# Performance work log

Measured on AMD Instinct MI355X. Metric: run time of the kernel, lower is better.

Reference implementation:

```python
import jax, jax.numpy as jnp
import numpy as np

B, F, H, W, C = 1, 16, 32, 32, 128


def setup_inputs() -> dict:
    key = jax.random.key(0)
    ks = jax.random.split(key, 6)
    w = lambda k: jax.random.normal(k, (C, C), jnp.float32) * 0.02
    return {
        "x": jax.random.normal(ks[0], (B, F, H, W, C), jnp.float32),
        "gamma": jnp.ones((C,), jnp.float32),
        "wq": w(ks[1]), "bq": jnp.zeros((C,), jnp.float32),
        "wk": w(ks[2]), "bk": jnp.zeros((C,), jnp.float32),
        "wv": w(ks[3]), "bv": jnp.zeros((C,), jnp.float32),
        "wo": w(ks[4]), "bo": jnp.zeros((C,), jnp.float32),
    }


def reference(x, gamma, wq, bq, wk, bk, wv, bv, wo, bo):
    b, f, h, w_, c = x.shape
    s, n_hw = f * h * w_, h * w_
    identity = x

    # RMSNorm variant: L2-normalize over channels, rescale by sqrt(C) * gamma
    xn = x / (jnp.linalg.norm(x, axis=-1, keepdims=True) + 1e-8)
    xn = xn * (c ** 0.5) * gamma

    # 1x1x1 convs == pointwise linear projections; flatten to tokens [b, s, c]
    xn = xn.reshape(b, s, c)
    q = xn @ wq + bq
    k = xn @ wk + bk
    v = xn @ wv + bv

    # frame-causal block mask: query at frame i attends to all keys in frames <= i
    frame = jnp.arange(s) // n_hw                      # [s]
    allowed = frame[:, None] >= frame[None, :]          # [s, s] bool

    scale = 1.0 / jnp.sqrt(c)
    scores = jnp.einsum('bqc,bkc->bqk', q, k) * scale   # [b, s, s]
    scores = jnp.where(allowed, scores, -jnp.inf)
    attn = jax.nn.softmax(scores, axis=-1)
    out = jnp.einsum('bqk,bkc->bqc', attn, v)           # [b, s, c]

    out = out @ wo + bo
    return out.reshape(b, f, h, w_, c) + identity
```

## Files before the change

### kernel.cpp

```cpp
#include <hip/hip_runtime.h>
#include <hip/hip_bf16.h>

typedef __bf16 bf16x8 __attribute__((ext_vector_type(8)));
typedef float f32x4 __attribute__((ext_vector_type(4)));
typedef float f32x16 __attribute__((ext_vector_type(16)));
typedef unsigned short u16;
typedef unsigned int u32;
typedef u16 ushort8 __attribute__((ext_vector_type(8)));
typedef u32 u32x4 __attribute__((ext_vector_type(4)));

#define S_TOK 16384
#define C_DIM 128
#define L2E 1.4426950408889634f
#define QK_SCALE 0.08838834764831845f
#define SQRTC 11.313708498984761f

#define NBLK 512
#define TPB 34

#define WT_OFF   0u
#define BIAS_OFF 131072u
#define XN_OFF   147456u
#define O_OFF    XN_OFF
#define Q_OFF    (XN_OFF + 4194304u)
#define K_OFF    (Q_OFF + 4194304u)
#define VF_OFF   (K_OFF + 4194304u)
#define PART_OFF (VF_OFF + 4194304u)
#define ML_OFF   (PART_OFF + 20971520u)

#define ZERO16 ((f32x16){0.f,0.f,0.f,0.f,0.f,0.f,0.f,0.f,0.f,0.f,0.f,0.f,0.f,0.f,0.f,0.f})

__device__ __forceinline__ int in_is_bf16(const void* gamma) {
  return ((const u16*)gamma)[0] == 0x3F80;
}
__device__ __forceinline__ float ldf(const void* p, int i, int bf) {
  if (bf) { u32 b = ((const u16*)p)[i]; return __uint_as_float(b << 16); }
  return ((const float*)p)[i];
}
__device__ __forceinline__ float b2f(u16 b) { return __uint_as_float((u32)b << 16); }
__device__ __forceinline__ u16 f2b(float f) {
  return __builtin_bit_cast(u16, (__bf16)f);
}
__device__ __forceinline__ float fexp2(float x) {
  float y; asm("v_exp_f32 %0, %1" : "=v"(y) : "v"(x)); return y;
}
__device__ __forceinline__ void gld16(const void* g, void* l) {
  __builtin_amdgcn_global_load_lds((const __attribute__((address_space(1))) u32*)g,
                                   (__attribute__((address_space(3))) u32*)l, 16, 0, 0);
}
__device__ __forceinline__ int qb_of(int t) {
  int F = 0;
  while (64 * (F + 1) * (F + 2) <= t) F++;
  int span = 16 * (F + 1);
  return 8 * F + (t - 64 * F * (F + 1)) / span;
}
__device__ __forceinline__ int start_of(int qq) {
  int Fq = qq >> 3, iq = qq & 7;
  return 16 * (Fq + 1) * (4 * Fq + iq);
}

__global__ void __launch_bounds__(256) prep_norm_kernel(const void* x, const void* gamma,
    const void* wq, const void* bq, const void* wk, const void* bk,
    const void* wv, const void* bv, const void* wo, const void* bo, char* ws) {
  int bf = in_is_bf16(gamma);
  if (blockIdx.x >= 2048) {
    int bb = blockIdx.x - 2048;
    if (bb < 256) {
      int gid = bb * 256 + threadIdx.x;
      int m = gid >> 14; int rem = gid & 16383;
      int k = rem >> 7; int n = rem & 127;
      const void* W = (m == 0) ? wq : (m == 1) ? wk : (m == 2) ? wv : wo;
      float v = ldf(W, rem, bf);
      if (m == 0) v *= QK_SCALE;
      *(u16*)(ws + WT_OFF + (u32)m * 32768u + (u32)n * 256u + (((u32)k * 2u) ^ (u32)((n & 7) << 4))) = f2b(v);
    } else {
      int idx = (bb - 256) * 256 + threadIdx.x;
      if (idx < 512) {
        int m = idx >> 7; int c = idx & 127;
        const void* B = (m == 0) ? bq : (m == 1) ? bk : (m == 2) ? bv : bo;
        float v = ldf(B, c, bf);
        if (m == 0) v *= QK_SCALE;
        ((float*)(ws + BIAS_OFF))[idx] = v;
      }
    }
    return;
  }
  int t = blockIdx.x * 256 + threadIdx.x;
  int tok = t >> 5; int sub = t & 31;
  int base = tok * 128 + sub * 4;
  float f[4];
  if (bf) {
    ushort4 v = ((const ushort4*)x)[base >> 2];
    f[0] = __uint_as_float((u32)v.x << 16); f[1] = __uint_as_float((u32)v.y << 16);
    f[2] = __uint_as_float((u32)v.z << 16); f[3] = __uint_as_float((u32)v.w << 16);
  } else {
    float4 v = ((const float4*)x)[base >> 2];
    f[0] = v.x; f[1] = v.y; f[2] = v.z; f[3] = v.w;
  }
  float ss = f[0]*f[0] + f[1]*f[1] + f[2]*f[2] + f[3]*f[3];
  #pragma unroll
  for (int m = 1; m < 32; m <<= 1) ss += __shfl_xor(ss, m);
  float fac = SQRTC / (sqrtf(ss) + 1e-8f);
  u16 o[4];
  #pragma unroll
  for (int j = 0; j < 4; j++) { float g = ldf(gamma, sub * 4 + j, bf); o[j] = f2b(f[j] * fac * g); }
  *(ushort4*)(ws + XN_OFF + (u32)tok * 256u + (((u32)sub * 8u) ^ (u32)((tok & 7) << 4))) =
      make_ushort4(o[0], o[1], o[2], o[3]);
}

__global__ void __launch_bounds__(256) qkv_kernel(char* ws) {
  __shared__ char lds[65536];
  int tid = threadIdx.x; int wid = tid >> 6; int lane = tid & 63;
  int blk = blockIdx.x & 127;
  int m = blockIdx.x >> 7;
  #pragma unroll
  for (int i = 0; i < 8; i++) {
    u32 seg = (u32)(i * 4 + wid) * 1024u;
    gld16(ws + XN_OFF + (u32)blk * 32768u + seg + (u32)lane * 16u, lds + seg);
    gld16(ws + WT_OFF + (u32)m * 32768u + seg + (u32)lane * 16u, lds + 32768 + seg);
  }
  __syncthreads();
  const float* bias = (const float*)(ws + BIAS_OFF);
  int rb = wid * 32;
  f32x4 acc[2][8];
  #pragma unroll
  for (int a = 0; a < 2; a++)
    #pragma unroll
    for (int b = 0; b < 8; b++) acc[a][b] = (f32x4){0.f, 0.f, 0.f, 0.f};
  #pragma unroll
  for (int kt = 0; kt < 4; kt++) {
    bf16x8 afr[2];
    #pragma unroll
    for (int mt = 0; mt < 2; mt++) {
      int row = rb + mt * 16 + (lane & 15);
      afr[mt] = *(const bf16x8*)(lds + row * 256 + ((kt * 64 + ((lane >> 4) * 16)) ^ ((row & 7) << 4)));
    }
    #pragma unroll
    for (int nt = 0; nt < 8; nt++) {
      int nr = nt * 16 + (lane & 15);
      bf16x8 bfr = *(const bf16x8*)(lds + 32768 + nr * 256 + ((kt * 64 + ((lane >> 4) * 16)) ^ ((nr & 7) << 4)));
      #pragma unroll
      for (int mt = 0; mt < 2; mt++)
        acc[mt][nt] = __builtin_amdgcn_mfma_f32_16x16x32_bf16(afr[mt], bfr, acc[mt][nt], 0, 0, 0);
    }
  }
  #pragma unroll
  for (int mt = 0; mt < 2; mt++)
    #pragma unroll
    for (int nt = 0; nt < 8; nt++) {
      int tok0 = blk * 128 + rb + mt * 16 + (lane >> 4) * 4;
      int c = (lane & 15) + nt * 16;
      float bv_ = bias[m * 128 + c];
      if (m == 0) {
        #pragma unroll
        for (int r = 0; r < 4; r++)
          *(u16*)(ws + Q_OFF + ((u32)(tok0 + r) * 128u + (u32)c) * 2u) = f2b(acc[mt][nt][r] + bv_);
      } else if (m == 1) {
        char* bp = ws + K_OFF + (u32)(tok0 >> 6) * 16384u
                 + (u32)((((tok0 >> 5) & 1) << 3) + (c >> 4)) * 1024u
                 + (u32)((tok0 & 31) + 32 * ((c >> 3) & 1)) * 16u + (u32)(c & 7) * 2u;
        #pragma unroll
        for (int r = 0; r < 4; r++)
          *(u16*)(bp + r * 16) = f2b(acc[mt][nt][r] + bv_);
      } else {
        u16 pk[4];
        #pragma unroll
        for (int r = 0; r < 4; r++) pk[r] = f2b(acc[mt][nt][r] + bv_);
        *(ushort4*)(ws + VF_OFF + (u32)(tok0 >> 6) * 16384u
                    + (u32)(((c >> 5) << 2) + ((tok0 >> 4) & 3)) * 1024u
                    + (u32)((c & 31) + 32 * ((tok0 >> 3) & 1)) * 16u + (u32)(tok0 & 7) * 2u)
            = make_ushort4(pk[0], pk[1], pk[2], pk[3]);
      }
    }
}

__global__ void __launch_bounds__(256, 2) attn_part_kernel(char* ws) {
  __shared__ char lds[65536];
  int tid = threadIdx.x; int wid = tid >> 6; int lane = tid & 63;
  int q = lane & 31; int hi = lane >> 5;
  int b = blockIdx.x;
  int slot = b;
  for (int qq = 1; qq < 128; qq++) {
    int Sx = start_of(qq);
    if (Sx < TPB * b && (Sx % TPB) != 0) slot++;
  }
  ushort8 ones_u;
  #pragma unroll
  for (int e = 0; e < 8; e++) ones_u[e] = 0x3F80;
  bf16x8 ones = __builtin_bit_cast(bf16x8, ones_u);

  auto stageK = [&](int t, int buf) {
    #pragma unroll
    for (int i = 0; i < 4; i++) {
      u32 off = (u32)(i * 4096) + (u32)tid * 16u;
      gld16(ws + K_OFF + (u32)t * 16384u + off, lds + buf * 16384 + off);
    }
  };
  auto stageV = [&](int t, int buf) {
    #pragma unroll
    for (int i = 0; i < 4; i++) {
      u32 off = (u32)(i * 4096) + (u32)tid * 16u;
      gld16(ws + VF_OFF + (u32)t * 16384u + off, lds + 32768 + buf * 16384 + off);
    }
  };

  int t0 = TPB * b, remaining = TPB;
  while (remaining > 0) {
    int F = 0;
    while (64 * (F + 1) * (F + 2) <= t0) F++;
    int fb = 64 * F * (F + 1); int span = 16 * (F + 1);
    int i = (t0 - fb) / span; int l = t0 - fb - i * span;
    int qb = 8 * F + i;
    int nt = min(remaining, span - l);

    bf16x8 aq[8];
    {
      const char* qp = ws + Q_OFF + (u32)(qb * 128 + wid * 32 + q) * 256u + (u32)(hi * 16);
      #pragma unroll
      for (int kt = 0; kt < 8; kt++) aq[kt] = *(const bf16x8*)(qp + kt * 32);
    }
    f32x16 acc0 = ZERO16, acc1 = ZERO16, acc2 = ZERO16, acc3 = ZERO16, accl = ZERO16;
    float m_run = -1e30f;
    float mL2 = m_run * L2E;

    __syncthreads();
    stageK(l, 0); stageV(l, 0);
    for (int it = 0; it < nt; it++) {
      int cur = it & 1;
      __syncthreads();
      if (it + 1 < nt) { stageK(l + it + 1, cur ^ 1); stageV(l + it + 1, cur ^ 1); }
      const char* kb_ = lds + cur * 16384;
      const char* vb_ = lds + 32768 + cur * 16384;
      f32x16 s0 = ZERO16, s1 = ZERO16;
      __builtin_amdgcn_s_setprio(1);
      #pragma unroll
      for (int kt = 0; kt < 8; kt++) {
        bf16x8 k0 = *(const bf16x8*)(kb_ + (0 * 8 + kt) * 1024 + (u32)lane * 16u);
        bf16x8 k1 = *(const bf16x8*)(kb_ + (1 * 8 + kt) * 1024 + (u32)lane * 16u);
        s0 = __builtin_amdgcn_mfma_f32_32x32x16_bf16(k0, aq[kt], s0, 0, 0, 0);
        s1 = __builtin_amdgcn_mfma_f32_32x32x16_bf16(k1, aq[kt], s1, 0, 0, 0);
      }
      __builtin_amdgcn_s_setprio(0);
      float tm = s0[0];
      #pragma unroll
      for (int r = 1; r < 16; r++) tm = fmaxf(tm, s0[r]);
      #pragma unroll
      for (int r = 0; r < 16; r++) tm = fmaxf(tm, s1[r]);
      tm = fmaxf(tm, __shfl_xor(tm, 32));
      if (__any(tm > m_run + 8.0f)) {
        float mnew = fmaxf(m_run, tm);
        float alpha = fexp2((m_run - mnew) * L2E);
        #pragma unroll
        for (int r = 0; r < 16; r++) {
          acc0[r] *= alpha; acc1[r] *= alpha; acc2[r] *= alpha; acc3[r] *= alpha; accl[r] *= alpha;
        }
        m_run = mnew; mL2 = m_run * L2E;
      }
      u32 W[16];
      #pragma unroll
      for (int t = 0; t < 8; t++) {
        float pa = fexp2(__builtin_fmaf(s0[2 * t], L2E, -mL2));
        float pb = fexp2(__builtin_fmaf(s0[2 * t + 1], L2E, -mL2));
        asm("v_cvt_pk_bf16_f32 %0, %1, %2" : "=v"(W[t]) : "v"(pa), "v"(pb));
      }
      #pragma unroll
      for (int t = 0; t < 8; t++) {
        float pa = fexp2(__builtin_fmaf(s1[2 * t], L2E, -mL2));
        float pb = fexp2(__builtin_fmaf(s1[2 * t + 1], L2E, -mL2));
        asm("v_cvt_pk_bf16_f32 %0, %1, %2" : "=v"(W[8 + t]) : "v"(pa), "v"(pb));
      }
      __builtin_amdgcn_s_setprio(1);
      #pragma unroll
      for (int kq = 0; kq < 4; kq++) {
        int base = (kq >> 1) * 8 + (kq & 1) * 4;
        u32 e0 = W[base + 0], e2 = W[base + 2];
        u32 e1 = W[base + 1], e3 = W[base + 3];
        asm("v_permlane32_swap_b32 %0, %1" : "+v"(e2), "+v"(e0));
        asm("v_permlane32_swap_b32 %0, %1" : "+v"(e3), "+v"(e1));
        u32x4 pw = (u32x4){e0, e1, e2, e3};
        bf16x8 pfr = __builtin_bit_cast(bf16x8, pw);
        accl = __builtin_amdgcn_mfma_f32_32x32x16_bf16(ones, pfr, accl, 0, 0, 0);
        bf16x8 v0 = *(const bf16x8*)(vb_ + (0 * 4 + kq) * 1024 + (u32)lane * 16u);
        bf16x8 v1 = *(const bf16x8*)(vb_ + (1 * 4 + kq) * 1024 + (u32)lane * 16u);
        bf16x8 v2 = *(const bf16x8*)(vb_ + (2 * 4 + kq) * 1024 + (u32)lane * 16u);
        bf16x8 v3 = *(const bf16x8*)(vb_ + (3 * 4 + kq) * 1024 + (u32)lane * 16u);
        acc0 = __builtin_amdgcn_mfma_f32_32x32x16_bf16(v0, pfr, acc0, 0, 0, 0);
        acc1 = __builtin_amdgcn_mfma_f32_32x32x16_bf16(v1, pfr, acc1, 0, 0, 0);
        acc2 = __builtin_amdgcn_mfma_f32_32x32x16_bf16(v2, pfr, acc2, 0, 0, 0);
        acc3 = __builtin_amdgcn_mfma_f32_32x32x16_bf16(v3, pfr, acc3, 0, 0, 0);
      }
      __builtin_amdgcn_s_setprio(0);
    }
    float l_run = accl[0];
    float rinv = 1.0f / l_run;
    int lrow = wid * 32 + q;
    char* pb2 = ws + PART_OFF + (u32)slot * 32768u + (u32)lrow * 256u;
    #pragma unroll
    for (int cb = 0; cb < 4; cb++) {
      const f32x16* A = (cb == 0) ? &acc0 : (cb == 1) ? &acc1 : (cb == 2) ? &acc2 : &acc3;
      #pragma unroll
      for (int t = 0; t < 8; t++) {
        float fa = (*A)[2 * t] * rinv, fb = (*A)[2 * t + 1] * rinv;
        u32 w;
        asm("v_cvt_pk_bf16_f32 %0, %1, %2" : "=v"(w) : "v"(fa), "v"(fb));
        int ch = cb * 32 + 8 * (t >> 1) + 2 * (t & 1) + 4 * hi;
        *(u32*)(pb2 + ch * 2) = w;
      }
    }
    if (hi == 0) ((float2*)(ws + ML_OFF))[slot * 128 + lrow] = make_float2(m_run, l_run);
    t0 += nt; remaining -= nt; slot++;
  }
}

__global__ void __launch_bounds__(256) combine_kernel(char* ws) {
  int qb = blockIdx.x >> 2;
  int seg = blockIdx.x & 3;
  int Sq = start_of(qb);
  int Eq = Sq + 16 * ((qb >> 3) + 1);
  int c_lo = Sq / TPB, c_hi = (Eq - 1) / TPB;
  int bse0 = c_lo;
  for (int qq = 1; qq < 128; qq++) {
    int Sx = start_of(qq);
    if (Sx < TPB * c_lo && (Sx % TPB) != 0) bse0++;
  }
  int tid = threadIdx.x;
  int row = seg * 32 + (tid >> 3);
  int oct = tid & 7;
  const float2* ml = (const float2*)(ws + ML_OFF);
  float M = -1e30f;
  {
    int bse = bse0;
    for (int c = c_lo; c <= c_hi; c++) {
      int qbf = qb_of(TPB * c);
      int qbl = qb_of(TPB * c + TPB - 1);
      int slot = bse + (qb - qbf);
      M = fmaxf(M, ml[slot * 128 + row].x);
      bse += qbl - qbf + 1;
    }
  }
  float a[16];
  #pragma unroll
  for (int k = 0; k < 16; k++) a[k] = 0.f;
  float D = 0.f;
  {
    int bse = bse0;
    for (int c = c_lo; c <= c_hi; c++) {
      int qbf = qb_of(TPB * c);
      int qbl = qb_of(TPB * c + TPB - 1);
      int slot = bse + (qb - qbf);
      bse += qbl - qbf + 1;
      float2 m_l = ml[slot * 128 + row];
      float w = exp2f((m_l.x - M) * L2E) * m_l.y;
      D += w;
      const u16* o = (const u16*)(ws + PART_OFF + (u32)slot * 32768u + (u32)row * 256u + (u32)oct * 32u);
      ushort8 v0 = *(const ushort8*)o;
      ushort8 v1 = *(const ushort8*)(o + 8);
      #pragma unroll
      for (int e = 0; e < 8; e++) { a[e] += w * b2f(v0[e]); a[8 + e] += w * b2f(v1[e]); }
    }
  }
  float Dinv = 1.0f / D;
  int grow = qb * 128 + row;
  ushort8 w0, w1;
  #pragma unroll
  for (int e = 0; e < 8; e++) { w0[e] = f2b(a[e] * Dinv); w1[e] = f2b(a[8 + e] * Dinv); }
  u32 rbase = (u32)grow * 256u;
  u32 swz = (u32)((row & 7) << 4);
  *(ushort8*)(ws + O_OFF + rbase + (((u32)oct * 32u) ^ swz)) = w0;
  *(ushort8*)(ws + O_OFF + rbase + (((u32)oct * 32u + 16u) ^ swz)) = w1;
}

__global__ void __launch_bounds__(256) out_kernel(const void* x, const void* gamma, char* ws, void* out) {
  __shared__ char lds[65536];
  int bf = in_is_bf16(gamma);
  int tid = threadIdx.x; int wid = tid >> 6; int lane = tid & 63;
  int blk = blockIdx.x;
  #pragma unroll
  for (int i = 0; i < 8; i++) {
    u32 seg = (u32)(i * 4 + wid) * 1024u;
    gld16(ws + O_OFF + (u32)blk * 32768u + seg + (u32)lane * 16u, lds + seg);
    gld16(ws + WT_OFF + 3u * 32768u + seg + (u32)lane * 16u, lds + 32768 + seg);
  }
  __syncthreads();
  f32x4 acc[2][8];
  #pragma unroll
  for (int a = 0; a < 2; a++)
    #pragma unroll
    for (int b = 0; b < 8; b++) acc[a][b] = (f32x4){0.f, 0.f, 0.f, 0.f};
  int rb = wid * 32;
  #pragma unroll
  for (int kt = 0; kt < 4; kt++) {
    bf16x8 afr[2];
    #pragma unroll
    for (int mt = 0; mt < 2; mt++) {
      int row = rb + mt * 16 + (lane & 15);
      afr[mt] = *(const bf16x8*)(lds + row * 256 + ((kt * 64 + ((lane >> 4) * 16)) ^ ((row & 7) << 4)));
    }
    #pragma unroll
    for (int nt = 0; nt < 8; nt++) {
      int nr = nt * 16 + (lane & 15);
      bf16x8 bfr = *(const bf16x8*)(lds + 32768 + nr * 256 + ((kt * 64 + ((lane >> 4) * 16)) ^ ((nr & 7) << 4)));
      #pragma unroll
      for (int mt = 0; mt < 2; mt++)
        acc[mt][nt] = __builtin_amdgcn_mfma_f32_16x16x32_bf16(afr[mt], bfr, acc[mt][nt], 0, 0, 0);
    }
  }
  const float* bias = (const float*)(ws + BIAS_OFF) + 3 * 128;
  #pragma unroll
  for (int mt = 0; mt < 2; mt++)
    #pragma unroll
    for (int nt = 0; nt < 8; nt++) {
      int c = (lane & 15) + nt * 16;
      float bv_ = bias[c];
      #pragma unroll
      for (int r = 0; r < 4; r++) {
        int tok = blk * 128 + rb + mt * 16 + (lane >> 4) * 4 + r;
        float v = acc[mt][nt][r] + bv_ + ldf(x, tok * 128 + c, bf);
        if (bf) ((u16*)out)[tok * 128 + c] = f2b(v);
        else    ((float*)out)[tok * 128 + c] = v;
      }
    }
}

extern "C" void kernel_launch(void* const* d_in, const int* in_sizes, int n_in,
                              void* d_out, int out_size, void* d_ws, size_t ws_size,
                              hipStream_t stream) {
  (void)in_sizes; (void)n_in; (void)out_size; (void)ws_size;
  const void* x     = d_in[0];
  const void* gamma = d_in[1];
  const void* wq = d_in[2]; const void* bq = d_in[3];
  const void* wk = d_in[4]; const void* bk = d_in[5];
  const void* wv = d_in[6]; const void* bv = d_in[7];
  const void* wo = d_in[8]; const void* bo = d_in[9];
  char* ws = (char*)d_ws;
  hipLaunchKernelGGL(prep_norm_kernel, dim3(2306), dim3(256), 0, stream,
                     x, gamma, wq, bq, wk, bk, wv, bv, wo, bo, ws);
  hipLaunchKernelGGL(qkv_kernel, dim3(384), dim3(256), 0, stream, ws);
  hipLaunchKernelGGL(attn_part_kernel, dim3(NBLK), dim3(256), 0, stream, ws);
  hipLaunchKernelGGL(combine_kernel, dim3(512), dim3(256), 0, stream, ws);
  hipLaunchKernelGGL(out_kernel, dim3(128), dim3(256), 0, stream, x, gamma, ws, d_out);
}
```

Measured before the change: 164.8 us.

## Fuse combine into output projection and compute softmax row sum on VALU

Merges the split-attention combine kernel into the output projection kernel. The merged normalized attention rows are written straight into LDS instead of round-tripping through the workspace, which removes one launch and a global write/read of O. The attention kernel also drops the extra ones-matrix MFMA used for the running row sum and accumulates the sum with VALU adds plus a cross-half shuffle. As a trade-off, the combine now runs on only 128 blocks, each handling 4 rows per thread, so it has less parallelism than the previous 512-block combine.

```diff
diff --git a/kernel.cpp b/kernel.cpp
--- a/kernel.cpp
+++ b/kernel.cpp
@@ -21,7 +21,6 @@
 #define WT_OFF   0u
 #define BIAS_OFF 131072u
 #define XN_OFF   147456u
-#define O_OFF    XN_OFF
 #define Q_OFF    (XN_OFF + 4194304u)
 #define K_OFF    (Q_OFF + 4194304u)
 #define VF_OFF   (K_OFF + 4194304u)
@@ -184,10 +183,6 @@
     int Sx = start_of(qq);
     if (Sx < TPB * b && (Sx % TPB) != 0) slot++;
   }
-  ushort8 ones_u;
-  #pragma unroll
-  for (int e = 0; e < 8; e++) ones_u[e] = 0x3F80;
-  bf16x8 ones = __builtin_bit_cast(bf16x8, ones_u);
 
   auto stageK = [&](int t, int buf) {
     #pragma unroll
@@ -219,8 +214,8 @@
       #pragma unroll
       for (int kt = 0; kt < 8; kt++) aq[kt] = *(const bf16x8*)(qp + kt * 32);
     }
-    f32x16 acc0 = ZERO16, acc1 = ZERO16, acc2 = ZERO16, acc3 = ZERO16, accl = ZERO16;
-    float m_run = -1e30f;
+    f32x16 acc0 = ZERO16, acc1 = ZERO16, acc2 = ZERO16, acc3 = ZERO16;
+    float m_run = -1e30f, l_run = 0.f;
     float mL2 = m_run * L2E;
 
     __syncthreads();
@@ -252,23 +247,29 @@
         float alpha = fexp2((m_run - mnew) * L2E);
         #pragma unroll
         for (int r = 0; r < 16; r++) {
-          acc0[r] *= alpha; acc1[r] *= alpha; acc2[r] *= alpha; acc3[r] *= alpha; accl[r] *= alpha;
+          acc0[r] *= alpha; acc1[r] *= alpha; acc2[r] *= alpha; acc3[r] *= alpha;
         }
+        l_run *= alpha;
         m_run = mnew; mL2 = m_run * L2E;
       }
       u32 W[16];
+      float ps = 0.f;
       #pragma unroll
       for (int t = 0; t < 8; t++) {
         float pa = fexp2(__builtin_fmaf(s0[2 * t], L2E, -mL2));
         float pb = fexp2(__builtin_fmaf(s0[2 * t + 1], L2E, -mL2));
+        ps += pa + pb;
         asm("v_cvt_pk_bf16_f32 %0, %1, %2" : "=v"(W[t]) : "v"(pa), "v"(pb));
       }
       #pragma unroll
       for (int t = 0; t < 8; t++) {
         float pa = fexp2(__builtin_fmaf(s1[2 * t], L2E, -mL2));
         float pb = fexp2(__builtin_fmaf(s1[2 * t + 1], L2E, -mL2));
+        ps += pa + pb;
         asm("v_cvt_pk_bf16_f32 %0, %1, %2" : "=v"(W[8 + t]) : "v"(pa), "v"(pb));
       }
+      ps += __shfl_xor(ps, 32);
+      l_run += ps;
       __builtin_amdgcn_s_setprio(1);
       #pragma unroll
       for (int kq = 0; kq < 4; kq++) {
@@ -279,7 +280,6 @@
         asm("v_permlane32_swap_b32 %0, %1" : "+v"(e3), "+v"(e1));
         u32x4 pw = (u32x4){e0, e1, e2, e3};
         bf16x8 pfr = __builtin_bit_cast(bf16x8, pw);
-        accl = __builtin_amdgcn_mfma_f32_32x32x16_bf16(ones, pfr, accl, 0, 0, 0);
         bf16x8 v0 = *(const bf16x8*)(vb_ + (0 * 4 + kq) * 1024 + (u32)lane * 16u);
         bf16x8 v1 = *(const bf16x8*)(vb_ + (1 * 4 + kq) * 1024 + (u32)lane * 16u);
         bf16x8 v2 = *(const bf16x8*)(vb_ + (2 * 4 + kq) * 1024 + (u32)lane * 16u);
@@ -291,7 +291,6 @@
       }
       __builtin_amdgcn_s_setprio(0);
     }
-    float l_run = accl[0];
     float rinv = 1.0f / l_run;
     int lrow = wid * 32 + q;
     char* pb2 = ws + PART_OFF + (u32)slot * 32768u + (u32)lrow * 256u;
@@ -312,9 +311,17 @@
   }
 }
 
-__global__ void __launch_bounds__(256) combine_kernel(char* ws) {
-  int qb = blockIdx.x >> 2;
-  int seg = blockIdx.x & 3;
+__global__ void __launch_bounds__(256) combine_out_kernel(const void* x, const void* gamma,
+                                                          char* ws, void* out) {
+  __shared__ char lds[65536];
+  int bf = in_is_bf16(gamma);
+  int tid = threadIdx.x; int wid = tid >> 6; int lane = tid & 63;
+  int qb = blockIdx.x;
+  #pragma unroll
+  for (int i = 0; i < 8; i++) {
+    u32 seg = (u32)(i * 4 + wid) * 1024u;
+    gld16(ws + WT_OFF + 3u * 32768u + seg + (u32)lane * 16u, lds + 32768 + seg);
+  }
   int Sq = start_of(qb);
   int Eq = Sq + 16 * ((qb >> 3) + 1);
   int c_lo = Sq / TPB, c_hi = (Eq - 1) / TPB;
@@ -323,63 +330,51 @@
     int Sx = start_of(qq);
     if (Sx < TPB * c_lo && (Sx % TPB) != 0) bse0++;
   }
-  int tid = threadIdx.x;
-  int row = seg * 32 + (tid >> 3);
   int oct = tid & 7;
+  int row0 = tid >> 3;
   const float2* ml = (const float2*)(ws + ML_OFF);
-  float M = -1e30f;
-  {
-    int bse = bse0;
-    for (int c = c_lo; c <= c_hi; c++) {
-      int qbf = qb_of(TPB * c);
-      int qbl = qb_of(TPB * c + TPB - 1);
-      int slot = bse + (qb - qbf);
-      M = fmaxf(M, ml[slot * 128 + row].x);
-      bse += qbl - qbf + 1;
-    }
-  }
-  float a[16];
-  #pragma unroll
-  for (int k = 0; k < 16; k++) a[k] = 0.f;
-  float D = 0.f;
-  {
-    int bse = bse0;
-    for (int c = c_lo; c <= c_hi; c++) {
-      int qbf = qb_of(TPB * c);
-      int qbl = qb_of(TPB * c + TPB - 1);
-      int slot = bse + (qb - qbf);
-      bse += qbl - qbf + 1;
-      float2 m_l = ml[slot * 128 + row];
-      float w = exp2f((m_l.x - M) * L2E) * m_l.y;
-      D += w;
-      const u16* o = (const u16*)(ws + PART_OFF + (u32)slot * 32768u + (u32)row * 256u + (u32)oct * 32u);
-      ushort8 v0 = *(const ushort8*)o;
-      ushort8 v1 = *(const ushort8*)(o + 8);
-      #pragma unroll
-      for (int e = 0; e < 8; e++) { a[e] += w * b2f(v0[e]); a[8 + e] += w * b2f(v1[e]); }
-    }
-  }
-  float Dinv = 1.0f / D;
-  int grow = qb * 128 + row;
-  ushort8 w0, w1;
-  #pragma unroll
-  for (int e = 0; e < 8; e++) { w0[e] = f2b(a[e] * Dinv); w1[e] = f2b(a[8 + e] * Dinv); }
-  u32 rbase = (u32)grow * 256u;
-  u32 swz = (u32)((row & 7) << 4);
-  *(ushort8*)(ws + O_OFF + rbase + (((u32)oct * 32u) ^ swz)) = w0;
-  *(ushort8*)(ws + O_OFF + rbase + (((u32)oct * 32u + 16u) ^ swz)) = w1;
-}
-
-__global__ void __launch_bounds__(256) out_kernel(const void* x, const void* gamma, char* ws, void* out) {
-  __shared__ char lds[65536];
-  int bf = in_is_bf16(gamma);
-  int tid = threadIdx.x; int wid = tid >> 6; int lane = tid & 63;
-  int blk = blockIdx.x;
-  #pragma unroll
-  for (int i = 0; i < 8; i++) {
-    u32 seg = (u32)(i * 4 + wid) * 1024u;
-    gld16(ws + O_OFF + (u32)blk * 32768u + seg + (u32)lane * 16u, lds + seg);
-    gld16(ws + WT_OFF + 3u * 32768u + seg + (u32)lane * 16u, lds + 32768 + seg);
+  for (int rr = 0; rr < 4; rr++) {
+    int row = row0 + rr * 32;
+    float M = -1e30f;
+    {
+      int bse = bse0;
+      for (int c = c_lo; c <= c_hi; c++) {
+        int qbf = qb_of(TPB * c);
+        int qbl = qb_of(TPB * c + TPB - 1);
+        int slot = bse + (qb - qbf);
+        M = fmaxf(M, ml[slot * 128 + row].x);
+        bse += qbl - qbf + 1;
+      }
+    }
+    float a[16];
+    #pragma unroll
+    for (int k = 0; k < 16; k++) a[k] = 0.f;
+    float D = 0.f;
+    {
+      int bse = bse0;
+      for (int c = c_lo; c <= c_hi; c++) {
+        int qbf = qb_of(TPB * c);
+        int qbl = qb_of(TPB * c + TPB - 1);
+        int slot = bse + (qb - qbf);
+        bse += qbl - qbf + 1;
+        float2 m_l = ml[slot * 128 + row];
+        float w = exp2f((m_l.x - M) * L2E) * m_l.y;
+        D += w;
+        const u16* o = (const u16*)(ws + PART_OFF + (u32)slot * 32768u + (u32)row * 256u + (u32)oct * 32u);
+        ushort8 v0 = *(const ushort8*)o;
+        ushort8 v1 = *(const ushort8*)(o + 8);
+        #pragma unroll
+        for (int e = 0; e < 8; e++) { a[e] += w * b2f(v0[e]); a[8 + e] += w * b2f(v1[e]); }
+      }
+    }
+    float Dinv = 1.0f / D;
+    ushort8 w0, w1;
+    #pragma unroll
+    for (int e = 0; e < 8; e++) { w0[e] = f2b(a[e] * Dinv); w1[e] = f2b(a[8 + e] * Dinv); }
+    u32 rbase = (u32)row * 256u;
+    u32 swz = (u32)((row & 7) << 4);
+    *(ushort8*)(lds + rbase + (((u32)oct * 32u) ^ swz)) = w0;
+    *(ushort8*)(lds + rbase + (((u32)oct * 32u + 16u) ^ swz)) = w1;
   }
   __syncthreads();
   f32x4 acc[2][8];
@@ -414,7 +409,7 @@
       float bv_ = bias[c];
       #pragma unroll
       for (int r = 0; r < 4; r++) {
-        int tok = blk * 128 + rb + mt * 16 + (lane >> 4) * 4 + r;
+        int tok = qb * 128 + rb + mt * 16 + (lane >> 4) * 4 + r;
         float v = acc[mt][nt][r] + bv_ + ldf(x, tok * 128 + c, bf);
         if (bf) ((u16*)out)[tok * 128 + c] = f2b(v);
         else    ((float*)out)[tok * 128 + c] = v;
@@ -437,6 +432,5 @@
                      x, gamma, wq, bq, wk, bk, wv, bv, wo, bo, ws);
   hipLaunchKernelGGL(qkv_kernel, dim3(384), dim3(256), 0, stream, ws);
   hipLaunchKernelGGL(attn_part_kernel, dim3(NBLK), dim3(256), 0, stream, ws);
-  hipLaunchKernelGGL(combine_kernel, dim3(512), dim3(256), 0, stream, ws);
-  hipLaunchKernelGGL(out_kernel, dim3(128), dim3(256), 0, stream, x, gamma, ws, d_out);
-}
+  hipLaunchKernelGGL(combine_out_kernel, dim3(128), dim3(256), 0, stream, x, gamma, ws, d_out);
+}
```

Measured after the change: 212.6 us. 1.29x slower.

## Double query rows per attention block to share staged K/V tiles across eight waves

Applied to the files above, without the earlier changes.

The attention-partial kernel now runs 512-thread blocks covering 256 query rows (a query superblock) instead of 128, and launches half as many blocks. Every K/V tile loaded into LDS is now consumed by eight waves instead of four, which halves global-to-LDS K/V traffic per unit of work. The work-split math, the partial/ML slot layout and the combine kernel's indexing are all rewritten for 256-row superblocks. The cost is fewer, larger blocks: a 128-VGPR budget per thread under the new launch bounds, and coarser load balancing with one block per CU.

```diff
diff --git a/kernel.cpp b/kernel.cpp
--- a/kernel.cpp
+++ b/kernel.cpp
@@ -15,7 +15,7 @@
 #define QK_SCALE 0.08838834764831845f
 #define SQRTC 11.313708498984761f
 
-#define NBLK 512
+#define NBLK 256
 #define TPB 34
 
 #define WT_OFF   0u
@@ -48,15 +48,15 @@
   __builtin_amdgcn_global_load_lds((const __attribute__((address_space(1))) u32*)g,
                                    (__attribute__((address_space(3))) u32*)l, 16, 0, 0);
 }
-__device__ __forceinline__ int qb_of(int t) {
+__device__ __forceinline__ int sb_of(int t) {
   int F = 0;
-  while (64 * (F + 1) * (F + 2) <= t) F++;
+  while (32 * (F + 1) * (F + 2) <= t) F++;
   int span = 16 * (F + 1);
-  return 8 * F + (t - 64 * F * (F + 1)) / span;
-}
-__device__ __forceinline__ int start_of(int qq) {
-  int Fq = qq >> 3, iq = qq & 7;
-  return 16 * (Fq + 1) * (4 * Fq + iq);
+  return 4 * F + (t - 32 * F * (F + 1)) / span;
+}
+__device__ __forceinline__ int sstart_of(int ss) {
+  int Fq = ss >> 2, iq = ss & 3;
+  return 16 * (Fq + 1) * (2 * Fq + iq);
 }
 
 __global__ void __launch_bounds__(256) prep_norm_kernel(const void* x, const void* gamma,
@@ -174,14 +174,14 @@
     }
 }
 
-__global__ void __launch_bounds__(256, 2) attn_part_kernel(char* ws) {
+__global__ void __launch_bounds__(512, 2) attn_part_kernel(char* ws) {
   __shared__ char lds[65536];
   int tid = threadIdx.x; int wid = tid >> 6; int lane = tid & 63;
   int q = lane & 31; int hi = lane >> 5;
   int b = blockIdx.x;
   int slot = b;
-  for (int qq = 1; qq < 128; qq++) {
-    int Sx = start_of(qq);
+  for (int ss = 1; ss < 64; ss++) {
+    int Sx = sstart_of(ss);
     if (Sx < TPB * b && (Sx % TPB) != 0) slot++;
   }
   ushort8 ones_u;
@@ -191,15 +191,15 @@
 
   auto stageK = [&](int t, int buf) {
     #pragma unroll
-    for (int i = 0; i < 4; i++) {
-      u32 off = (u32)(i * 4096) + (u32)tid * 16u;
+    for (int i = 0; i < 2; i++) {
+      u32 off = (u32)(i * 8192) + (u32)tid * 16u;
       gld16(ws + K_OFF + (u32)t * 16384u + off, lds + buf * 16384 + off);
     }
   };
   auto stageV = [&](int t, int buf) {
     #pragma unroll
-    for (int i = 0; i < 4; i++) {
-      u32 off = (u32)(i * 4096) + (u32)tid * 16u;
+    for (int i = 0; i < 2; i++) {
+      u32 off = (u32)(i * 8192) + (u32)tid * 16u;
       gld16(ws + VF_OFF + (u32)t * 16384u + off, lds + 32768 + buf * 16384 + off);
     }
   };
@@ -207,15 +207,15 @@
   int t0 = TPB * b, remaining = TPB;
   while (remaining > 0) {
     int F = 0;
-    while (64 * (F + 1) * (F + 2) <= t0) F++;
-    int fb = 64 * F * (F + 1); int span = 16 * (F + 1);
+    while (32 * (F + 1) * (F + 2) <= t0) F++;
+    int fb = 32 * F * (F + 1); int span = 16 * (F + 1);
     int i = (t0 - fb) / span; int l = t0 - fb - i * span;
-    int qb = 8 * F + i;
+    int sb = 4 * F + i;
     int nt = min(remaining, span - l);
 
     bf16x8 aq[8];
     {
-      const char* qp = ws + Q_OFF + (u32)(qb * 128 + wid * 32 + q) * 256u + (u32)(hi * 16);
+      const char* qp = ws + Q_OFF + (u32)(sb * 256 + wid * 32 + q) * 256u + (u32)(hi * 16);
       #pragma unroll
       for (int kt = 0; kt < 8; kt++) aq[kt] = *(const bf16x8*)(qp + kt * 32);
     }
@@ -294,7 +294,7 @@
     float l_run = accl[0];
     float rinv = 1.0f / l_run;
     int lrow = wid * 32 + q;
-    char* pb2 = ws + PART_OFF + (u32)slot * 32768u + (u32)lrow * 256u;
+    char* pb2 = ws + PART_OFF + (u32)slot * 65536u + (u32)lrow * 256u;
     #pragma unroll
     for (int cb = 0; cb < 4; cb++) {
       const f32x16* A = (cb == 0) ? &acc0 : (cb == 1) ? &acc1 : (cb == 2) ? &acc2 : &acc3;
@@ -307,20 +307,21 @@
         *(u32*)(pb2 + ch * 2) = w;
       }
     }
-    if (hi == 0) ((float2*)(ws + ML_OFF))[slot * 128 + lrow] = make_float2(m_run, l_run);
+    if (hi == 0) ((float2*)(ws + ML_OFF))[slot * 256 + lrow] = make_float2(m_run, l_run);
     t0 += nt; remaining -= nt; slot++;
   }
 }
 
 __global__ void __launch_bounds__(256) combine_kernel(char* ws) {
-  int qb = blockIdx.x >> 2;
-  int seg = blockIdx.x & 3;
-  int Sq = start_of(qb);
-  int Eq = Sq + 16 * ((qb >> 3) + 1);
+  int sb = blockIdx.x >> 3;
+  int seg = blockIdx.x & 7;
+  int F = sb >> 2;
+  int Sq = sstart_of(sb);
+  int Eq = Sq + 16 * (F + 1);
   int c_lo = Sq / TPB, c_hi = (Eq - 1) / TPB;
   int bse0 = c_lo;
-  for (int qq = 1; qq < 128; qq++) {
-    int Sx = start_of(qq);
+  for (int ss = 1; ss < 64; ss++) {
+    int Sx = sstart_of(ss);
     if (Sx < TPB * c_lo && (Sx % TPB) != 0) bse0++;
   }
   int tid = threadIdx.x;
@@ -331,11 +332,11 @@
   {
     int bse = bse0;
     for (int c = c_lo; c <= c_hi; c++) {
-      int qbf = qb_of(TPB * c);
-      int qbl = qb_of(TPB * c + TPB - 1);
-      int slot = bse + (qb - qbf);
-      M = fmaxf(M, ml[slot * 128 + row].x);
-      bse += qbl - qbf + 1;
+      int sbf = sb_of(TPB * c);
+      int sbl = sb_of(TPB * c + TPB - 1);
+      int slot = bse + (sb - sbf);
+      M = fmaxf(M, ml[slot * 256 + row].x);
+      bse += sbl - sbf + 1;
     }
   }
   float a[16];
@@ -345,14 +346,14 @@
   {
     int bse = bse0;
     for (int c = c_lo; c <= c_hi; c++) {
-      int qbf = qb_of(TPB * c);
-      int qbl = qb_of(TPB * c + TPB - 1);
-      int slot = bse + (qb - qbf);
-      bse += qbl - qbf + 1;
-      float2 m_l = ml[slot * 128 + row];
+      int sbf = sb_of(TPB * c);
+      int sbl = sb_of(TPB * c + TPB - 1);
+      int slot = bse + (sb - sbf);
+      bse += sbl - sbf + 1;
+      float2 m_l = ml[slot * 256 + row];
       float w = exp2f((m_l.x - M) * L2E) * m_l.y;
       D += w;
-      const u16* o = (const u16*)(ws + PART_OFF + (u32)slot * 32768u + (u32)row * 256u + (u32)oct * 32u);
+      const u16* o = (const u16*)(ws + PART_OFF + (u32)slot * 65536u + (u32)row * 256u + (u32)oct * 32u);
       ushort8 v0 = *(const ushort8*)o;
       ushort8 v1 = *(const ushort8*)(o + 8);
       #pragma unroll
@@ -360,7 +361,7 @@
     }
   }
   float Dinv = 1.0f / D;
-  int grow = qb * 128 + row;
+  int grow = sb * 256 + row;
   ushort8 w0, w1;
   #pragma unroll
   for (int e = 0; e < 8; e++) { w0[e] = f2b(a[e] * Dinv); w1[e] = f2b(a[8 + e] * Dinv); }
@@ -436,7 +437,7 @@
   hipLaunchKernelGGL(prep_norm_kernel, dim3(2306), dim3(256), 0, stream,
                      x, gamma, wq, bq, wk, bk, wv, bv, wo, bo, ws);
   hipLaunchKernelGGL(qkv_kernel, dim3(384), dim3(256), 0, stream, ws);
-  hipLaunchKernelGGL(attn_part_kernel, dim3(NBLK), dim3(256), 0, stream, ws);
+  hipLaunchKernelGGL(attn_part_kernel, dim3(NBLK), dim3(512), 0, stream, ws);
   hipLaunchKernelGGL(combine_kernel, dim3(512), dim3(256), 0, stream, ws);
   hipLaunchKernelGGL(out_kernel, dim3(128), dim3(256), 0, stream, x, gamma, ws, d_out);
 }
```

After: 148.8 us, median of 2. 9.7% less time.
